# Performance work log

Hardware: AMD Instinct MI355X
Metric: run time of the kernel (lower is better)

The kernel has to match this reference:

```python
import jax, jax.numpy as jnp
import numpy as np

BS, T, Q, HID, PROJ = 16, 16, 100, 256, 256


def setup_inputs() -> dict:
    key = jax.random.key(0)
    k1, k2, k3, k4, k5 = jax.random.split(key, 5)
    frame_embeds = jax.random.normal(k1, (BS, T, Q, HID), jnp.float32)
    other_frame_embeds = jax.random.normal(k2, (BS, T, Q, HID), jnp.float32)
    W = jax.random.normal(k3, (HID, PROJ), jnp.float32) / np.sqrt(HID).astype(np.float32)
    b = jax.random.normal(k4, (PROJ,), jnp.float32) * 0.01
    n = BS * Q
    mid = jax.random.randint(k5, (n, 1), 1, T - 1, dtype=jnp.int32)
    bridge = jnp.concatenate(
        [jnp.zeros((n, 1), jnp.int32), mid, jnp.full((n, 1), T - 1, jnp.int32)], axis=1
    )  # (n,3): head=0, random pivot in [1,T-2], tail=T-1
    return {"frame_embeds": frame_embeds, "other_frame_embeds": other_frame_embeds,
            "W": W, "b": b, "bridge": bridge}


def _prep(fe, W, b):
    # Linear proj, (bs,t,q,c)->(bs*q, t, c), L2-normalize per embedding.
    bs, t, q, _ = fe.shape
    x = fe @ W + b
    x = x.transpose(0, 2, 1, 3).reshape(bs * q, t, -1)
    return x / jnp.linalg.norm(x, axis=-1, keepdims=True)


def _forward(frame_embeds, other_frame_embeds, W, b, bridge, delta=0.3):
    cur = _prep(frame_embeds, W, b)      # (n,t,c)
    other = _prep(other_frame_embeds, W, b)
    bh = bridge[:, 0].astype(jnp.float32)
    bp_f = bridge[:, 1].astype(jnp.float32)
    bt = bridge[:, 2].astype(jnp.float32)
    alpha = (bp_f - bh) / (bt - bh)      # (n,)
    sigma = alpha * (bt - bp_f)          # (n,)
    g = jnp.take_along_axis(cur, bridge[:, :, None], axis=1)  # (n,3,c) head/pivot/tail
    # positive brownian-bridge distance
    x = g[:, 1] - (1.0 - alpha)[:, None] * g[:, 0] - alpha[:, None] * g[:, 2]
    numer = jnp.exp(-jnp.sum(x * x, axis=-1) / (2.0 * sigma ** 2))  # (n,)
    # negatives: pivot frame taken from every sequence in [cur; other].
    # ||m_ij - a_i||^2 = ||m_ij||^2 - 2 m_ij.a_i + ||a_i||^2 with m_ij = neg_all[j, bp_i],
    # avoiding the (n,N,3,c) repeat tensor of the original.
    neg_all = jnp.concatenate([cur, other], axis=0)            # (N,t,c)
    a = (1.0 - alpha)[:, None] * g[:, 0] + alpha[:, None] * g[:, 2]  # (n,c)
    cross = jnp.einsum('ic,jtc->ijt', a, neg_all)              # (n,N,t)
    bp = bridge[:, 1]
    cross_g = jnp.take_along_axis(cross, bp[:, None, None], axis=2)[..., 0]  # (n,N)
    nn2_g = jnp.sum(neg_all * neg_all, axis=-1).T[bp]          # (n,N)
    x2 = nn2_g - 2.0 * cross_g + jnp.sum(a * a, axis=-1)[:, None]
    dist = -x2 / (2.0 * sigma ** 2)[:, None]                   # (n,N)
    n = dist.shape[0]
    idx = jnp.arange(n)
    self_dist = dist[idx, idx]
    dist = dist.at[idx, idx].set(-10000.0)
    topv, _ = jax.lax.top_k(dist, 5)
    deno = jnp.exp(jnp.concatenate([self_dist[:, None], topv], axis=-1))  # (n,6)
    brownian_loss = (numer / deno.sum(axis=-1)).mean()
    score = jnp.einsum('nc,nc->n', cur[:, 0], cur[:, -1])
    head_tail_match = jax.nn.softplus(delta - score).mean()
    return brownian_loss, head_tail_match


def reference(frame_embeds, other_frame_embeds, W, b, bridge):
    return _forward(frame_embeds, other_frame_embeds, W, b, bridge)
```

## Files before the change

### kernel.cpp

```cpp
#include <hip/hip_runtime.h>
#include <hip/hip_bf16.h>

#define NROW 1600
#define NEG  3200
#define ROWS_FLAT 25600
#define NSPLIT 25

using bf16x8 = __attribute__((ext_vector_type(8))) short;
using f32x4  = __attribute__((ext_vector_type(4))) float;

__device__ __forceinline__ float bf2f(unsigned v) { return __uint_as_float(v << 16); }
__device__ __forceinline__ ushort f2bf(float f) {
  __hip_bfloat16 h = __float2bfloat16(f);
  return *(ushort*)&h;
}
__device__ __forceinline__ float load1(const ushort* p, size_t idx, int f32) {
  return f32 ? ((const float*)p)[idx] : bf2f(p[idx]);
}
__device__ __forceinline__ void load8(const ushort* p, size_t idx, int f32, float* o) {
  if (f32) {
    const float* q = (const float*)p;
    float4 a = *(const float4*)(q + idx);
    float4 b = *(const float4*)(q + idx + 4);
    o[0]=a.x; o[1]=a.y; o[2]=a.z; o[3]=a.w;
    o[4]=b.x; o[5]=b.y; o[6]=b.z; o[7]=b.w;
  } else {
    uint4 u = *(const uint4*)(p + idx);
    o[0]=bf2f(u.x & 0xffffu); o[1]=bf2f(u.x >> 16);
    o[2]=bf2f(u.y & 0xffffu); o[3]=bf2f(u.y >> 16);
    o[4]=bf2f(u.z & 0xffffu); o[5]=bf2f(u.z >> 16);
    o[6]=bf2f(u.w & 0xffffu); o[7]=bf2f(u.w >> 16);
  }
}
__device__ __forceinline__ int sniff_f32(const ushort* p, int lane) {
  unsigned e = ((unsigned)p[2*lane] >> 7) & 0xffu;
  unsigned long long b = __ballot(e >= 100u && e <= 140u);
  return (__popcll(b) >= 40) ? 0 : 1;
}

__global__ __launch_bounds__(256) void k_prepw(const ushort* __restrict__ W,
    ushort* __restrict__ Wt, int* __restrict__ zbase) {
  if (blockIdx.x == 0 && threadIdx.x < 21) zbase[threadIdx.x] = 0;
  int fW = sniff_f32(W, threadIdx.x & 63);
  int n = blockIdx.x, k = threadIdx.x;
  Wt[n*256 + k] = f2bf(load1(W, (size_t)k*256 + n, fW));
}

__global__ __launch_bounds__(256) void k_proj(const ushort* __restrict__ fe0,
    const ushort* __restrict__ fe1, const ushort* __restrict__ Wt,
    const ushort* __restrict__ bias, ushort* __restrict__ Pb) {
  __shared__ union {
    ushort x[64*256];
    ushort c[4][32*72];
  } sh;
  __shared__ float s_ss[4][64];
  const int tid = threadIdx.x;
  const int w = tid >> 6, lane = tid & 63, q = lane >> 4, m = lane & 15;
  const int grow0 = blockIdx.x * 64;
  const int src1 = (grow0 >= ROWS_FLAT);
  const ushort* src = src1 ? fe1 : fe0;
  const size_t rbase = (size_t)(src1 ? grow0 - ROWS_FLAT : grow0) * 256;
  const int fSrc = sniff_f32(src, lane);
  const int fB   = sniff_f32(bias, lane);
  if (!fSrc) {
    #pragma unroll
    for (int i = 0; i < 8; i++) {
      int c = w*8 + i;
      int r = 2*c + (lane >> 5);
      int kc = (lane & 31) ^ (r & 7);
      const ushort* gp = src + rbase + (size_t)r*256 + kc*8;
      __builtin_amdgcn_global_load_lds(
        (const __attribute__((address_space(1))) unsigned int*)gp,
        (__attribute__((address_space(3))) unsigned int*)&sh.x[c*512],
        16, 0, 0);
    }
  } else {
    #pragma unroll
    for (int i = 0; i < 8; i++) {
      int l = tid + i*256;
      int r = l >> 5, kc = l & 31;
      float o[8];
      load8(src, rbase + (size_t)r*256 + kc*8, 1, o);
      uint4 u;
      u.x = (unsigned)f2bf(o[0]) | ((unsigned)f2bf(o[1]) << 16);
      u.y = (unsigned)f2bf(o[2]) | ((unsigned)f2bf(o[3]) << 16);
      u.z = (unsigned)f2bf(o[4]) | ((unsigned)f2bf(o[5]) << 16);
      u.w = (unsigned)f2bf(o[6]) | ((unsigned)f2bf(o[7]) << 16);
      *(uint4*)&sh.x[r*256 + ((kc*8) ^ ((r&7)<<3))] = u;
    }
  }
  __syncthreads();
  f32x4 acc[4][4];
  #pragma unroll
  for (int nt = 0; nt < 4; nt++) {
    float bb = load1(bias, w*64 + nt*16 + m, fB);
    f32x4 v = {bb, bb, bb, bb};
    #pragma unroll
    for (int mt = 0; mt < 4; mt++) acc[mt][nt] = v;
  }
  const int sw = (m & 7) << 3;
  const ushort* wbase = Wt + (size_t)(w*64 + m)*256 + q*8;
  bf16x8 a_cur[4], b_cur[4];
  #pragma unroll
  for (int mt = 0; mt < 4; mt++)
    a_cur[mt] = *(const bf16x8*)&sh.x[(mt*16 + m)*256 + ((q*8) ^ sw)];
  #pragma unroll
  for (int nt = 0; nt < 4; nt++)
    b_cur[nt] = *(const bf16x8*)(wbase + (size_t)nt*16*256);
  #pragma unroll
  for (int k = 0; k < 8; k++) {
    bf16x8 a_nxt[4], b_nxt[4];
    if (k < 7) {
      int k0 = (k + 1) * 32;
      #pragma unroll
      for (int nt = 0; nt < 4; nt++)
        b_nxt[nt] = *(const bf16x8*)(wbase + (size_t)nt*16*256 + k0);
      int pk = (k0 + q*8) ^ sw;
      #pragma unroll
      for (int mt = 0; mt < 4; mt++)
        a_nxt[mt] = *(const bf16x8*)&sh.x[(mt*16 + m)*256 + pk];
    }
    #pragma unroll
    for (int nt = 0; nt < 4; nt++)
      #pragma unroll
      for (int mt = 0; mt < 4; mt++)
        acc[mt][nt] = __builtin_amdgcn_mfma_f32_16x16x32_bf16(a_cur[mt], b_cur[nt], acc[mt][nt], 0, 0, 0);
    if (k < 7) {
      #pragma unroll
      for (int x = 0; x < 4; x++) { a_cur[x] = a_nxt[x]; b_cur[x] = b_nxt[x]; }
    }
  }
  float ssp[4][4];
  #pragma unroll
  for (int mt = 0; mt < 4; mt++)
    #pragma unroll
    for (int reg = 0; reg < 4; reg++) {
      float s = 0.f;
      #pragma unroll
      for (int nt = 0; nt < 4; nt++) { float v = acc[mt][nt][reg]; s += v*v; }
      ssp[mt][reg] = s;
    }
  #pragma unroll
  for (int mk = 1; mk < 16; mk <<= 1)
    #pragma unroll
    for (int mt = 0; mt < 4; mt++)
      #pragma unroll
      for (int reg = 0; reg < 4; reg++) ssp[mt][reg] += __shfl_xor(ssp[mt][reg], mk, 64);
  if (m == 0)
    #pragma unroll
    for (int mt = 0; mt < 4; mt++)
      #pragma unroll
      for (int reg = 0; reg < 4; reg++) s_ss[w][mt*16 + 4*q + reg] = ssp[mt][reg];
  __syncthreads();
  float inv[4][4];
  #pragma unroll
  for (int mt = 0; mt < 4; mt++)
    #pragma unroll
    for (int reg = 0; reg < 4; reg++) {
      int row = mt*16 + 4*q + reg;
      float s = s_ss[0][row] + s_ss[1][row] + s_ss[2][row] + s_ss[3][row];
      inv[mt][reg] = 1.0f / sqrtf(s);
    }
  #pragma unroll
  for (int half = 0; half < 2; half++) {
    #pragma unroll
    for (int mt = half*2; mt < half*2 + 2; mt++)
      #pragma unroll
      for (int reg = 0; reg < 4; reg++) {
        int rl = (mt - half*2)*16 + 4*q + reg;
        #pragma unroll
        for (int nt = 0; nt < 4; nt++)
          sh.c[w][rl*72 + nt*16 + m] = f2bf(acc[mt][nt][reg] * inv[mt][reg]);
      }
    int rl = (lane >> 3), c16 = lane & 7;
    #pragma unroll
    for (int it = 0; it < 4; it++) {
      int row = it*8 + rl;
      int grow = grow0 + half*32 + row;
      int srcid = grow / ROWS_FLAT;
      int rem   = grow % ROWS_FLAT;
      int b  = rem / 1600;
      int t  = (rem / 100) & 15;
      int qq = rem % 100;
      size_t orow = ((size_t)(srcid*1600 + b*100 + qq) * 16 + t) * 256;
      uint4 v = *(uint4*)&sh.c[w][row*72 + c16*8];
      *(uint4*)(Pb + orow + w*64 + c16*8) = v;
    }
  }
}

__global__ __launch_bounds__(256) void k_bridge(const ushort* __restrict__ Pb,
    const int* __restrict__ bridge, ushort* __restrict__ Ab,
    float* __restrict__ prm, float* __restrict__ numer,
    int* __restrict__ cnt, int* __restrict__ lst, float* __restrict__ wsum) {
  int i = blockIdx.x, c = threadIdx.x;
  int bh = bridge[i*3+0], bp = bridge[i*3+1], bt = bridge[i*3+2];
  float bhf = (float)bh, bpf = (float)bp, btf = (float)bt;
  float alpha = (bpf - bhf) / (btf - bhf);
  float sigma = alpha * (btf - bpf);
  const ushort* base = Pb + (size_t)i * 16 * 256;
  float g0 = bf2f(base[bh*256 + c]), g1 = bf2f(base[bp*256 + c]), g2 = bf2f(base[bt*256 + c]);
  float head = bf2f(base[c]), tail = bf2f(base[15*256 + c]);
  float a = (1.0f - alpha) * g0 + alpha * g2;
  float x = g1 - a;
  Ab[(size_t)i*256 + c] = f2bf(a);
  float xx = x*x, aac = a*a, sc = head*tail;
  #pragma unroll
  for (int mk = 1; mk < 64; mk <<= 1) {
    xx  += __shfl_xor(xx, mk, 64);
    aac += __shfl_xor(aac, mk, 64);
    sc  += __shfl_xor(sc, mk, 64);
  }
  __shared__ float red[3][4];
  int wv = c >> 6;
  if ((c & 63) == 0) { red[0][wv]=xx; red[1][wv]=aac; red[2][wv]=sc; }
  __syncthreads();
  if (c == 0) {
    float XX = red[0][0]+red[0][1]+red[0][2]+red[0][3];
    float AA = red[1][0]+red[1][1]+red[1][2]+red[1][3];
    float SC = red[2][0]+red[2][1]+red[2][2]+red[2][3];
    float inv2s2 = 1.0f / (2.0f * sigma * sigma);
    prm[i*2+0] = inv2s2;
    prm[i*2+1] = AA;
    numer[i] = expf(-XX * inv2s2);
    float sp = log1pf(expf(0.3f - SC));
    atomicAdd(wsum + 1, sp * (1.0f / 1600.0f));
    int pos = atomicAdd(cnt + bp, 1);
    lst[bp * 1600 + pos] = i;
  }
}

__device__ __forceinline__ void sort5(float* c) {
  #define CE(i,j) { float hi = fmaxf(c[i], c[j]), lo = fminf(c[i], c[j]); c[i]=hi; c[j]=lo; }
  CE(0,1) CE(3,4) CE(2,4) CE(2,3) CE(1,4) CE(0,3) CE(0,2) CE(1,3) CE(1,2)
  #undef CE
}
__device__ __forceinline__ void ins5(float* t, float v) {
  float hi, lo;
  hi = fmaxf(t[0], v); lo = fminf(t[0], v); t[0] = hi; v = lo;
  hi = fmaxf(t[1], v); lo = fminf(t[1], v); t[1] = hi; v = lo;
  hi = fmaxf(t[2], v); lo = fminf(t[2], v); t[2] = hi; v = lo;
  hi = fmaxf(t[3], v); lo = fminf(t[3], v); t[3] = hi; v = lo;
  t[4] = fmaxf(t[4], v);
}

__global__ __launch_bounds__(256) void k_cross(const ushort* __restrict__ Pb,
    const ushort* __restrict__ Ab, const float* __restrict__ prm,
    const int* __restrict__ cnt, const int* __restrict__ lst,
    float* __restrict__ part) {
  int t = blockIdx.z;
  int n_t = min(cnt[t], 1600);
  int i0 = blockIdx.y * 64;
  if (i0 >= n_t) return;
  int j0 = blockIdx.x * 128;
  __shared__ int s_gis[64];
  __shared__ float s_red[4][64][6];
  int tid = threadIdx.x;
  if (tid < 64) {
    int gi = lst[t*1600 + min(i0 + tid, n_t - 1)];
    s_gis[tid] = min(max(gi, 0), NROW - 1);
  }
  __syncthreads();
  const int w = tid >> 6, lane = tid & 63, q = lane >> 4, m = lane & 15;
  const ushort* jp0 = Pb + ((size_t)(j0 + w*32 + m)*16 + t) * 256 + q*8;
  const ushort* jp1 = jp0 + (size_t)16*16*256;
  int gi[4];
  const ushort* ip[4];
  #pragma unroll
  for (int it = 0; it < 4; it++) {
    gi[it] = s_gis[it*16 + m];
    ip[it] = Ab + (size_t)gi[it] * 256 + q*8;
  }
  f32x4 acc[2][4];
  #pragma unroll
  for (int jt = 0; jt < 2; jt++)
    #pragma unroll
    for (int it = 0; it < 4; it++) { f32x4 z = {0.f,0.f,0.f,0.f}; acc[jt][it] = z; }
  bf16x8 jc0 = *(const bf16x8*)(jp0);
  bf16x8 jc1 = *(const bf16x8*)(jp1);
  bf16x8 ic[4];
  #pragma unroll
  for (int it = 0; it < 4; it++) ic[it] = *(const bf16x8*)(ip[it]);
  #pragma unroll
  for (int k = 0; k < 8; k++) {
    bf16x8 jn0, jn1, in[4];
    if (k < 7) {
      int o = (k + 1) * 32;
      jn0 = *(const bf16x8*)(jp0 + o);
      jn1 = *(const bf16x8*)(jp1 + o);
      #pragma unroll
      for (int it = 0; it < 4; it++) in[it] = *(const bf16x8*)(ip[it] + o);
    }
    #pragma unroll
    for (int it = 0; it < 4; it++) {
      acc[0][it] = __builtin_amdgcn_mfma_f32_16x16x32_bf16(jc0, ic[it], acc[0][it], 0, 0, 0);
      acc[1][it] = __builtin_amdgcn_mfma_f32_16x16x32_bf16(jc1, ic[it], acc[1][it], 0, 0, 0);
    }
    if (k < 7) { jc0 = jn0; jc1 = jn1;
      #pragma unroll
      for (int it = 0; it < 4; it++) ic[it] = in[it];
    }
  }
  float top[4][5], selfv[4];
  float pi[4], pa[4];
  #pragma unroll
  for (int it = 0; it < 4; it++) {
    pi[it] = prm[gi[it]*2]; pa[it] = prm[gi[it]*2+1];
    selfv[it] = -1e30f;
    #pragma unroll
    for (int k = 0; k < 5; k++) top[it][k] = -1e30f;
  }
  #pragma unroll
  for (int jt = 0; jt < 2; jt++)
    #pragma unroll
    for (int reg = 0; reg < 4; reg++) {
      int j = j0 + w*32 + jt*16 + 4*q + reg;
      #pragma unroll
      for (int it = 0; it < 4; it++) {
        float d = -(1.0f - 2.0f*acc[jt][it][reg] + pa[it]) * pi[it];
        if (j == gi[it]) selfv[it] = d; else ins5(top[it], d);
      }
    }
  #pragma unroll
  for (int mk = 16; mk <= 32; mk <<= 1) {
    #pragma unroll
    for (int it = 0; it < 4; it++) {
      float o[5], c[5];
      #pragma unroll
      for (int k = 0; k < 5; k++) o[k] = __shfl_xor(top[it][k], mk, 64);
      #pragma unroll
      for (int k = 0; k < 5; k++) c[k] = fmaxf(top[it][k], o[4 - k]);
      sort5(c);
      #pragma unroll
      for (int k = 0; k < 5; k++) top[it][k] = c[k];
      selfv[it] = fmaxf(selfv[it], __shfl_xor(selfv[it], mk, 64));
    }
  }
  if (q == 0) {
    #pragma unroll
    for (int it = 0; it < 4; it++) {
      #pragma unroll
      for (int k = 0; k < 5; k++) s_red[w][it*16 + m][k] = top[it][k];
      s_red[w][it*16 + m][5] = selfv[it];
    }
  }
  __syncthreads();
  if (tid < 64 && i0 + tid < n_t) {
    float T[5], S = s_red[0][tid][5];
    #pragma unroll
    for (int k = 0; k < 5; k++) T[k] = s_red[0][tid][k];
    #pragma unroll
    for (int w2 = 1; w2 < 4; w2++) {
      #pragma unroll
      for (int k = 0; k < 5; k++) ins5(T, s_red[w2][tid][k]);
      S = fmaxf(S, s_red[w2][tid][5]);
    }
    float* pp = part + ((size_t)s_gis[tid]*NSPLIT + blockIdx.x) * 6;
    #pragma unroll
    for (int k = 0; k < 5; k++) pp[k] = T[k];
    pp[5] = S;
  }
}

__global__ __launch_bounds__(64) void k_merge(const float* __restrict__ part,
    const float* __restrict__ numer, float* __restrict__ wsum, int* __restrict__ done,
    const ushort* __restrict__ fe0, void* __restrict__ out) {
  int i = blockIdx.x * 64 + threadIdx.x;
  const float* pp = part + (size_t)i * NSPLIT * 6;
  float T[5]; float S = pp[5];
  #pragma unroll
  for (int k = 0; k < 5; k++) T[k] = pp[k];
  #pragma unroll
  for (int s = 1; s < NSPLIT; s++) {
    const float* ps = pp + s*6;
    float v0 = ps[0], v1 = ps[1], v2 = ps[2], v3 = ps[3], v4 = ps[4], v5 = ps[5];
    ins5(T, v0); ins5(T, v1); ins5(T, v2); ins5(T, v3); ins5(T, v4);
    S = fmaxf(S, v5);
  }
  float deno = expf(S);
  #pragma unroll
  for (int k = 0; k < 5; k++) deno += expf(T[k]);
  float local = numer[i] / deno;
  #pragma unroll
  for (int mk = 1; mk < 64; mk <<= 1) local += __shfl_xor(local, mk, 64);
  __shared__ int s_last;
  if (threadIdx.x == 0) {
    atomicAdd(wsum + 0, local * (1.0f / 1600.0f));
    __threadfence();
    s_last = (atomicAdd(done, 1) == 24);
  }
  __syncthreads();
  if (s_last) {
    int f = sniff_f32(fe0, threadIdx.x);
    if (threadIdx.x == 0) {
      __threadfence();
      float brown = __hip_atomic_load(wsum + 0, __ATOMIC_RELAXED, __HIP_MEMORY_SCOPE_AGENT);
      float sp    = __hip_atomic_load(wsum + 1, __ATOMIC_RELAXED, __HIP_MEMORY_SCOPE_AGENT);
      if (f) {
        ((float*)out)[0] = brown;
        ((float*)out)[1] = sp;
      } else {
        ushort* o = (ushort*)out;
        o[0] = f2bf(brown);
        o[1] = f2bf(sp);
      }
    }
  }
}

extern "C" void kernel_launch(void* const* d_in, const int* in_sizes, int n_in,
                              void* d_out, int out_size, void* d_ws, size_t ws_size,
                              hipStream_t stream) {
  const ushort* fe0    = (const ushort*)d_in[0];
  const ushort* fe1    = (const ushort*)d_in[1];
  const ushort* W      = (const ushort*)d_in[2];
  const ushort* bias   = (const ushort*)d_in[3];
  const int*    bridge = (const int*)d_in[4];

  ushort* Pb    = (ushort*)d_ws;
  ushort* Ab    = Pb + 13107200;
  ushort* Wt    = Ab + 409600;
  float*  part  = (float*)(Wt + 65536);
  float*  prm   = part + 240000;
  float*  numer = prm + 3200;
  float*  wsum  = numer + 1600;
  int*    cnt   = (int*)(wsum + 4);
  int*    done  = cnt + 16;
  int*    lst   = done + 1;

  k_prepw <<<256, 256, 0, stream>>>(W, Wt, (int*)wsum);
  k_proj  <<<800, 256, 0, stream>>>(fe0, fe1, Wt, bias, Pb);
  k_bridge<<<1600, 256, 0, stream>>>(Pb, bridge, Ab, prm, numer, cnt, lst, wsum);
  k_cross <<<dim3(NSPLIT, 7, 16), 256, 0, stream>>>(Pb, Ab, prm, cnt, lst, part);
  k_merge <<<25, 64, 0, stream>>>(part, numer, wsum, done, fe0, d_out);
}
```

Measured before the change: 191.2 us.

## Store projections t-major, bucket bridge rows by pivot, widen cross tile

The projection output is now stored time-major, so the negatives for one pivot frame form a contiguous block of rows. The bridge kernel writes the interpolated anchors and their parameters into per-pivot buckets, letting the cross kernel load them contiguously instead of gathering them through an index list. The cross kernel's tile now covers 128 anchor rows instead of 64, which halves how often negatives are reloaded but raises register use. The W transpose also goes through LDS so both its reads and writes are coalesced.

```diff
diff --git a/kernel.cpp b/kernel.cpp
--- a/kernel.cpp
+++ b/kernel.cpp
@@ -40,10 +40,18 @@
 
 __global__ __launch_bounds__(256) void k_prepw(const ushort* __restrict__ W,
     ushort* __restrict__ Wt, int* __restrict__ zbase) {
+  __shared__ float ld[16][257];
   if (blockIdx.x == 0 && threadIdx.x < 21) zbase[threadIdx.x] = 0;
   int fW = sniff_f32(W, threadIdx.x & 63);
-  int n = blockIdx.x, k = threadIdx.x;
-  Wt[n*256 + k] = f2bf(load1(W, (size_t)k*256 + n, fW));
+  int k0 = blockIdx.x * 16, tid = threadIdx.x;
+  #pragma unroll
+  for (int r = 0; r < 16; r++) ld[r][tid] = load1(W, (size_t)(k0 + r)*256 + tid, fW);
+  __syncthreads();
+  ushort buf[16];
+  #pragma unroll
+  for (int r = 0; r < 16; r++) buf[r] = f2bf(ld[r][tid]);
+  *(uint4*)(Wt + (size_t)tid*256 + k0)     = *(uint4*)&buf[0];
+  *(uint4*)(Wt + (size_t)tid*256 + k0 + 8) = *(uint4*)&buf[8];
 }
 
 __global__ __launch_bounds__(256) void k_proj(const ushort* __restrict__ fe0,
@@ -182,7 +190,7 @@
       int b  = rem / 1600;
       int t  = (rem / 100) & 15;
       int qq = rem % 100;
-      size_t orow = ((size_t)(srcid*1600 + b*100 + qq) * 16 + t) * 256;
+      size_t orow = ((size_t)t*3200 + srcid*1600 + b*100 + qq) * 256;
       uint4 v = *(uint4*)&sh.c[w][row*72 + c16*8];
       *(uint4*)(Pb + orow + w*64 + c16*8) = v;
     }
@@ -190,20 +198,21 @@
 }
 
 __global__ __launch_bounds__(256) void k_bridge(const ushort* __restrict__ Pb,
-    const int* __restrict__ bridge, ushort* __restrict__ Ab,
-    float* __restrict__ prm, float* __restrict__ numer,
+    const int* __restrict__ bridge, ushort* __restrict__ Ab_s,
+    float* __restrict__ prm_s, float* __restrict__ numer,
     int* __restrict__ cnt, int* __restrict__ lst, float* __restrict__ wsum) {
   int i = blockIdx.x, c = threadIdx.x;
   int bh = bridge[i*3+0], bp = bridge[i*3+1], bt = bridge[i*3+2];
   float bhf = (float)bh, bpf = (float)bp, btf = (float)bt;
   float alpha = (bpf - bhf) / (btf - bhf);
   float sigma = alpha * (btf - bpf);
-  const ushort* base = Pb + (size_t)i * 16 * 256;
-  float g0 = bf2f(base[bh*256 + c]), g1 = bf2f(base[bp*256 + c]), g2 = bf2f(base[bt*256 + c]);
-  float head = bf2f(base[c]), tail = bf2f(base[15*256 + c]);
+  float g0 = bf2f(Pb[((size_t)bh*3200 + i)*256 + c]);
+  float g1 = bf2f(Pb[((size_t)bp*3200 + i)*256 + c]);
+  float g2 = bf2f(Pb[((size_t)bt*3200 + i)*256 + c]);
+  float head = bf2f(Pb[(size_t)i*256 + c]);
+  float tail = bf2f(Pb[((size_t)15*3200 + i)*256 + c]);
   float a = (1.0f - alpha) * g0 + alpha * g2;
   float x = g1 - a;
-  Ab[(size_t)i*256 + c] = f2bf(a);
   float xx = x*x, aac = a*a, sc = head*tail;
   #pragma unroll
   for (int mk = 1; mk < 64; mk <<= 1) {
@@ -212,6 +221,7 @@
     sc  += __shfl_xor(sc, mk, 64);
   }
   __shared__ float red[3][4];
+  __shared__ int s_pos;
   int wv = c >> 6;
   if ((c & 63) == 0) { red[0][wv]=xx; red[1][wv]=aac; red[2][wv]=sc; }
   __syncthreads();
@@ -220,14 +230,17 @@
     float AA = red[1][0]+red[1][1]+red[1][2]+red[1][3];
     float SC = red[2][0]+red[2][1]+red[2][2]+red[2][3];
     float inv2s2 = 1.0f / (2.0f * sigma * sigma);
-    prm[i*2+0] = inv2s2;
-    prm[i*2+1] = AA;
     numer[i] = expf(-XX * inv2s2);
     float sp = log1pf(expf(0.3f - SC));
     atomicAdd(wsum + 1, sp * (1.0f / 1600.0f));
     int pos = atomicAdd(cnt + bp, 1);
+    s_pos = pos;
     lst[bp * 1600 + pos] = i;
-  }
+    prm_s[(bp*1600 + pos)*2 + 0] = inv2s2;
+    prm_s[(bp*1600 + pos)*2 + 1] = AA;
+  }
+  __syncthreads();
+  Ab_s[((size_t)bp*1600 + s_pos)*256 + c] = f2bf(a);
 }
 
 __device__ __forceinline__ void sort5(float* c) {
@@ -245,67 +258,72 @@
 }
 
 __global__ __launch_bounds__(256) void k_cross(const ushort* __restrict__ Pb,
-    const ushort* __restrict__ Ab, const float* __restrict__ prm,
+    const ushort* __restrict__ Ab_s, const float* __restrict__ prm_s,
     const int* __restrict__ cnt, const int* __restrict__ lst,
     float* __restrict__ part) {
   int t = blockIdx.z;
   int n_t = min(cnt[t], 1600);
-  int i0 = blockIdx.y * 64;
+  int i0 = blockIdx.y * 128;
   if (i0 >= n_t) return;
   int j0 = blockIdx.x * 128;
-  __shared__ int s_gis[64];
-  __shared__ float s_red[4][64][6];
+  __shared__ int s_gis[128];
+  __shared__ float s_red[4][128][6];
   int tid = threadIdx.x;
-  if (tid < 64) {
+  if (tid < 128) {
     int gi = lst[t*1600 + min(i0 + tid, n_t - 1)];
     s_gis[tid] = min(max(gi, 0), NROW - 1);
   }
   __syncthreads();
   const int w = tid >> 6, lane = tid & 63, q = lane >> 4, m = lane & 15;
-  const ushort* jp0 = Pb + ((size_t)(j0 + w*32 + m)*16 + t) * 256 + q*8;
-  const ushort* jp1 = jp0 + (size_t)16*16*256;
-  int gi[4];
-  const ushort* ip[4];
-  #pragma unroll
-  for (int it = 0; it < 4; it++) {
-    gi[it] = s_gis[it*16 + m];
-    ip[it] = Ab + (size_t)gi[it] * 256 + q*8;
-  }
-  f32x4 acc[2][4];
+  const ushort* jp[2];
   #pragma unroll
   for (int jt = 0; jt < 2; jt++)
-    #pragma unroll
-    for (int it = 0; it < 4; it++) { f32x4 z = {0.f,0.f,0.f,0.f}; acc[jt][it] = z; }
-  bf16x8 jc0 = *(const bf16x8*)(jp0);
-  bf16x8 jc1 = *(const bf16x8*)(jp1);
-  bf16x8 ic[4];
-  #pragma unroll
-  for (int it = 0; it < 4; it++) ic[it] = *(const bf16x8*)(ip[it]);
+    jp[jt] = Pb + ((size_t)t*3200 + j0 + w*32 + jt*16 + m)*256 + q*8;
+  int irow[8];
+  const ushort* ip[8];
+  #pragma unroll
+  for (int it = 0; it < 8; it++) {
+    irow[it] = min(i0 + it*16 + m, 1599);
+    ip[it] = Ab_s + ((size_t)t*1600 + irow[it])*256 + q*8;
+  }
+  f32x4 acc[2][8];
+  #pragma unroll
+  for (int jt = 0; jt < 2; jt++)
+    #pragma unroll
+    for (int it = 0; it < 8; it++) { f32x4 z = {0.f,0.f,0.f,0.f}; acc[jt][it] = z; }
+  bf16x8 jc[2], ic[8];
+  #pragma unroll
+  for (int jt = 0; jt < 2; jt++) jc[jt] = *(const bf16x8*)(jp[jt]);
+  #pragma unroll
+  for (int it = 0; it < 8; it++) ic[it] = *(const bf16x8*)(ip[it]);
   #pragma unroll
   for (int k = 0; k < 8; k++) {
-    bf16x8 jn0, jn1, in[4];
+    bf16x8 jn[2], in[8];
     if (k < 7) {
       int o = (k + 1) * 32;
-      jn0 = *(const bf16x8*)(jp0 + o);
-      jn1 = *(const bf16x8*)(jp1 + o);
-      #pragma unroll
-      for (int it = 0; it < 4; it++) in[it] = *(const bf16x8*)(ip[it] + o);
-    }
-    #pragma unroll
-    for (int it = 0; it < 4; it++) {
-      acc[0][it] = __builtin_amdgcn_mfma_f32_16x16x32_bf16(jc0, ic[it], acc[0][it], 0, 0, 0);
-      acc[1][it] = __builtin_amdgcn_mfma_f32_16x16x32_bf16(jc1, ic[it], acc[1][it], 0, 0, 0);
-    }
-    if (k < 7) { jc0 = jn0; jc1 = jn1;
-      #pragma unroll
-      for (int it = 0; it < 4; it++) ic[it] = in[it];
-    }
-  }
-  float top[4][5], selfv[4];
-  float pi[4], pa[4];
-  #pragma unroll
-  for (int it = 0; it < 4; it++) {
-    pi[it] = prm[gi[it]*2]; pa[it] = prm[gi[it]*2+1];
+      #pragma unroll
+      for (int jt = 0; jt < 2; jt++) jn[jt] = *(const bf16x8*)(jp[jt] + o);
+      #pragma unroll
+      for (int it = 0; it < 8; it++) in[it] = *(const bf16x8*)(ip[it] + o);
+    }
+    #pragma unroll
+    for (int it = 0; it < 8; it++) {
+      acc[0][it] = __builtin_amdgcn_mfma_f32_16x16x32_bf16(jc[0], ic[it], acc[0][it], 0, 0, 0);
+      acc[1][it] = __builtin_amdgcn_mfma_f32_16x16x32_bf16(jc[1], ic[it], acc[1][it], 0, 0, 0);
+    }
+    if (k < 7) {
+      jc[0] = jn[0]; jc[1] = jn[1];
+      #pragma unroll
+      for (int it = 0; it < 8; it++) ic[it] = in[it];
+    }
+  }
+  float top[8][5], selfv[8], pi[8], pa[8];
+  int gi[8];
+  #pragma unroll
+  for (int it = 0; it < 8; it++) {
+    pi[it] = prm_s[(t*1600 + irow[it])*2];
+    pa[it] = prm_s[(t*1600 + irow[it])*2 + 1];
+    gi[it] = s_gis[it*16 + m];
     selfv[it] = -1e30f;
     #pragma unroll
     for (int k = 0; k < 5; k++) top[it][k] = -1e30f;
@@ -316,7 +334,7 @@
     for (int reg = 0; reg < 4; reg++) {
       int j = j0 + w*32 + jt*16 + 4*q + reg;
       #pragma unroll
-      for (int it = 0; it < 4; it++) {
+      for (int it = 0; it < 8; it++) {
         float d = -(1.0f - 2.0f*acc[jt][it][reg] + pa[it]) * pi[it];
         if (j == gi[it]) selfv[it] = d; else ins5(top[it], d);
       }
@@ -324,7 +342,7 @@
   #pragma unroll
   for (int mk = 16; mk <= 32; mk <<= 1) {
     #pragma unroll
-    for (int it = 0; it < 4; it++) {
+    for (int it = 0; it < 8; it++) {
       float o[5], c[5];
       #pragma unroll
       for (int k = 0; k < 5; k++) o[k] = __shfl_xor(top[it][k], mk, 64);
@@ -338,14 +356,14 @@
   }
   if (q == 0) {
     #pragma unroll
-    for (int it = 0; it < 4; it++) {
+    for (int it = 0; it < 8; it++) {
       #pragma unroll
       for (int k = 0; k < 5; k++) s_red[w][it*16 + m][k] = top[it][k];
       s_red[w][it*16 + m][5] = selfv[it];
     }
   }
   __syncthreads();
-  if (tid < 64 && i0 + tid < n_t) {
+  if (tid < 128 && i0 + tid < n_t) {
     float T[5], S = s_red[0][tid][5];
     #pragma unroll
     for (int k = 0; k < 5; k++) T[k] = s_red[0][tid][k];
@@ -418,19 +436,19 @@
   const int*    bridge = (const int*)d_in[4];
 
   ushort* Pb    = (ushort*)d_ws;
-  ushort* Ab    = Pb + 13107200;
-  ushort* Wt    = Ab + 409600;
+  ushort* Ab_s  = Pb + 13107200;
+  ushort* Wt    = Ab_s + 6553600;
   float*  part  = (float*)(Wt + 65536);
-  float*  prm   = part + 240000;
-  float*  numer = prm + 3200;
+  float*  prm_s = part + 240000;
+  float*  numer = prm_s + 51200;
   float*  wsum  = numer + 1600;
   int*    cnt   = (int*)(wsum + 4);
   int*    done  = cnt + 16;
   int*    lst   = done + 1;
 
-  k_prepw <<<256, 256, 0, stream>>>(W, Wt, (int*)wsum);
+  k_prepw <<<16, 256, 0, stream>>>(W, Wt, (int*)wsum);
   k_proj  <<<800, 256, 0, stream>>>(fe0, fe1, Wt, bias, Pb);
-  k_bridge<<<1600, 256, 0, stream>>>(Pb, bridge, Ab, prm, numer, cnt, lst, wsum);
-  k_cross <<<dim3(NSPLIT, 7, 16), 256, 0, stream>>>(Pb, Ab, prm, cnt, lst, part);
+  k_bridge<<<1600, 256, 0, stream>>>(Pb, bridge, Ab_s, prm_s, numer, cnt, lst, wsum);
+  k_cross <<<dim3(NSPLIT, 13, 16), 256, 0, stream>>>(Pb, Ab_s, prm_s, cnt, lst, part);
   k_merge <<<25, 64, 0, stream>>>(part, numer, wsum, done, fe0, d_out);
 }
```

Measured after the change: 196.0 us. 2.5% more time.
